# Performance work log

Measured on AMD Instinct MI355X. Metric: run time of the kernel, lower is better.

Reference implementation:

```python
import jax, jax.numpy as jnp
import numpy as np

N_NEURONS = 1024
TABLE_SIZE = 65536  # array_size (2048 quotients) * 2**remainder_size (32)
BATCH = 8192


def setup_inputs() -> dict:
    key = jax.random.key(0)
    k1, k2 = jax.random.split(key)
    # Input tuples: one fingerprint per neuron per sample, value = (quotient << rs) | remainder
    data = jax.random.randint(k1, (BATCH, N_NEURONS), 0, TABLE_SIZE, dtype=jnp.int32)
    # Dense membership/counter table equivalent to the fitted quotient filter state
    # (quotient filter with full remainders stored is an exact fingerprint set).
    table = jax.random.uniform(k2, (N_NEURONS, TABLE_SIZE), dtype=jnp.float32)
    return {"data": data, "table": table}


def reference(data, table):
    # check_member(neuron=j, quotient=data[i,j]>>rs, remainder=data[i,j]&mask)
    # == table[j, data[i,j]]; multi_rank sums memberships over neurons.
    neuron_idx = jnp.arange(table.shape[0])[None, :]          # [1, N]
    gathered = table[neuron_idx, data]                        # [B, N] gather
    response = jnp.sum(gathered, axis=1)                      # [B]
    return response
```

## Files before the change

kernel.cpp:

```cpp
#include <hip/hip_runtime.h>

#define N_NEURONS 1024
#define TABLE_SIZE 65536
#define BATCH 8192
#define NGROUPS 8
#define NPG 128
#define HALF 64
#define SPB 128

__global__ __launch_bounds__(256) void qw_partial_kernel(
    const int* __restrict__ data,
    const float* __restrict__ table,
    float* __restrict__ part)
{
    const int b      = blockIdx.x;
    const int g      = b & (NGROUPS - 1);
    const int sub    = b >> 3;
    const int t      = threadIdx.x;
    const int half   = t >> 7;
    const int sid    = t & (SPB - 1);
    const int sample = sub * SPB + sid;
    const int jbase  = g * NPG + half * HALF;

    const int* __restrict__ drow = data + (size_t)sample * N_NEURONS + jbase;

    float acc = 0.0f;
#pragma unroll
    for (int jo = 0; jo < HALF; jo += 16) {
        const int4 i0 = *reinterpret_cast<const int4*>(drow + jo);
        const int4 i1 = *reinterpret_cast<const int4*>(drow + jo + 4);
        const int4 i2 = *reinterpret_cast<const int4*>(drow + jo + 8);
        const int4 i3 = *reinterpret_cast<const int4*>(drow + jo + 12);
        const float* __restrict__ tp = table + (size_t)(jbase + jo) * TABLE_SIZE;
        const float v0  = tp[(size_t) 0 * TABLE_SIZE + i0.x];
        const float v1  = tp[(size_t) 1 * TABLE_SIZE + i0.y];
        const float v2  = tp[(size_t) 2 * TABLE_SIZE + i0.z];
        const float v3  = tp[(size_t) 3 * TABLE_SIZE + i0.w];
        const float v4  = tp[(size_t) 4 * TABLE_SIZE + i1.x];
        const float v5  = tp[(size_t) 5 * TABLE_SIZE + i1.y];
        const float v6  = tp[(size_t) 6 * TABLE_SIZE + i1.z];
        const float v7  = tp[(size_t) 7 * TABLE_SIZE + i1.w];
        const float v8  = tp[(size_t) 8 * TABLE_SIZE + i2.x];
        const float v9  = tp[(size_t) 9 * TABLE_SIZE + i2.y];
        const float v10 = tp[(size_t)10 * TABLE_SIZE + i2.z];
        const float v11 = tp[(size_t)11 * TABLE_SIZE + i2.w];
        const float v12 = tp[(size_t)12 * TABLE_SIZE + i3.x];
        const float v13 = tp[(size_t)13 * TABLE_SIZE + i3.y];
        const float v14 = tp[(size_t)14 * TABLE_SIZE + i3.z];
        const float v15 = tp[(size_t)15 * TABLE_SIZE + i3.w];
        acc += (((v0 + v1) + (v2 + v3)) + ((v4 + v5) + (v6 + v7)))
             + (((v8 + v9) + (v10 + v11)) + ((v12 + v13) + (v14 + v15)));
    }

    __shared__ float lds[SPB];
    if (half == 0) {
        lds[sid] = acc;
    }
    __syncthreads();
    if (half == 1) {
        part[(size_t)g * BATCH + sample] = lds[sid] + acc;
    }
}

__global__ __launch_bounds__(256) void qw_reduce_kernel(
    const float* __restrict__ part,
    float* __restrict__ out)
{
    const int i = blockIdx.x * 256 + threadIdx.x;
    float s = 0.0f;
#pragma unroll
    for (int g = 0; g < NGROUPS; ++g) {
        s += part[(size_t)g * BATCH + i];
    }
    out[i] = s;
}

__global__ __launch_bounds__(256) void qw_gather_kernel(
    const int* __restrict__ data,
    const float* __restrict__ table,
    float* __restrict__ out)
{
    const int gtid   = blockIdx.x * blockDim.x + threadIdx.x;
    const int sample = gtid >> 6;
    const int lane   = threadIdx.x & 63;
    if (sample >= BATCH) return;
    const int* __restrict__ row = data + (size_t)sample * N_NEURONS;
    float acc = 0.0f;
#pragma unroll
    for (int k = 0; k < 4; ++k) {
        const int jb = 256 * k + 4 * lane;
        const int4 idx4 = *reinterpret_cast<const int4*>(row + jb);
        acc += table[(size_t)(jb + 0) * TABLE_SIZE + idx4.x];
        acc += table[(size_t)(jb + 1) * TABLE_SIZE + idx4.y];
        acc += table[(size_t)(jb + 2) * TABLE_SIZE + idx4.z];
        acc += table[(size_t)(jb + 3) * TABLE_SIZE + idx4.w];
    }
#pragma unroll
    for (int off = 32; off >= 1; off >>= 1) acc += __shfl_xor(acc, off, 64);
    if (lane == 0) out[sample] = acc;
}

extern "C" void kernel_launch(void* const* d_in, const int* in_sizes, int n_in,
                              void* d_out, int out_size, void* d_ws, size_t ws_size,
                              hipStream_t stream)
{
    const int*   data  = (const int*)d_in[0];
    const float* table = (const float*)d_in[1];
    float*       out   = (float*)d_out;

    const size_t need = (size_t)NGROUPS * BATCH * sizeof(float);
    if (ws_size >= need) {
        float* part = (float*)d_ws;
        qw_partial_kernel<<<(BATCH / SPB) * NGROUPS, 256, 0, stream>>>(data, table, part);
        qw_reduce_kernel<<<BATCH / 256, 256, 0, stream>>>(part, out);
    } else {
        qw_gather_kernel<<<BATCH / 4, 256, 0, stream>>>(data, table, out);
    }
}
```

Measured before the change: 91.78 us.

## Split each sample across 4 lanes with interleaved neuron columns and shuffle reduction

The partial kernel now assigns 4 adjacent threads per sample, each covering interleaved groups of 4 neurons within the 128-neuron group. All index loads are issued up front, and the table gathers are software-pipelined with two register sets. A 2-step shuffle reduction replaces the LDS exchange and __syncthreads. Adjacent lanes now read contiguous index memory and hit neighbouring table rows, which changes coalescing and cache locality, and each block covers half as many samples, so the grid doubles.

```diff
diff --git a/kernel.cpp b/kernel.cpp
--- a/kernel.cpp
+++ b/kernel.cpp
@@ -5,8 +5,8 @@
 #define BATCH 8192
 #define NGROUPS 8
 #define NPG 128
-#define HALF 64
-#define SPB 128
+#define SPB 64
+#define TPS 4
 
 __global__ __launch_bounds__(256) void qw_partial_kernel(
     const int* __restrict__ data,
@@ -17,48 +17,49 @@
     const int g      = b & (NGROUPS - 1);
     const int sub    = b >> 3;
     const int t      = threadIdx.x;
-    const int half   = t >> 7;
-    const int sid    = t & (SPB - 1);
+    const int q      = t & (TPS - 1);
+    const int sid    = t >> 2;
     const int sample = sub * SPB + sid;
-    const int jbase  = g * NPG + half * HALF;
 
-    const int* __restrict__ drow = data + (size_t)sample * N_NEURONS + jbase;
+    const int* __restrict__ dptr =
+        data + (size_t)sample * N_NEURONS + g * NPG + q * 4;
+    const int4 idx0 = *reinterpret_cast<const int4*>(dptr + 0 * 16);
+    const int4 idx1 = *reinterpret_cast<const int4*>(dptr + 1 * 16);
+    const int4 idx2 = *reinterpret_cast<const int4*>(dptr + 2 * 16);
+    const int4 idx3 = *reinterpret_cast<const int4*>(dptr + 3 * 16);
+    const int4 idx4 = *reinterpret_cast<const int4*>(dptr + 4 * 16);
+    const int4 idx5 = *reinterpret_cast<const int4*>(dptr + 5 * 16);
+    const int4 idx6 = *reinterpret_cast<const int4*>(dptr + 6 * 16);
+    const int4 idx7 = *reinterpret_cast<const int4*>(dptr + 7 * 16);
 
+    const float* __restrict__ tb =
+        table + (size_t)(g * NPG + q * 4) * TABLE_SIZE;
+
+#define LOADC(a0, a1, a2, a3, I, c)                                   \
+    a0 = tb[(size_t)((c) * 16 + 0) * TABLE_SIZE + (size_t)(I).x];     \
+    a1 = tb[(size_t)((c) * 16 + 1) * TABLE_SIZE + (size_t)(I).y];     \
+    a2 = tb[(size_t)((c) * 16 + 2) * TABLE_SIZE + (size_t)(I).z];     \
+    a3 = tb[(size_t)((c) * 16 + 3) * TABLE_SIZE + (size_t)(I).w];
+
+    float v0, v1, v2, v3, w0, w1, w2, w3;
     float acc = 0.0f;
-#pragma unroll
-    for (int jo = 0; jo < HALF; jo += 16) {
-        const int4 i0 = *reinterpret_cast<const int4*>(drow + jo);
-        const int4 i1 = *reinterpret_cast<const int4*>(drow + jo + 4);
-        const int4 i2 = *reinterpret_cast<const int4*>(drow + jo + 8);
-        const int4 i3 = *reinterpret_cast<const int4*>(drow + jo + 12);
-        const float* __restrict__ tp = table + (size_t)(jbase + jo) * TABLE_SIZE;
-        const float v0  = tp[(size_t) 0 * TABLE_SIZE + i0.x];
-        const float v1  = tp[(size_t) 1 * TABLE_SIZE + i0.y];
-        const float v2  = tp[(size_t) 2 * TABLE_SIZE + i0.z];
-        const float v3  = tp[(size_t) 3 * TABLE_SIZE + i0.w];
-        const float v4  = tp[(size_t) 4 * TABLE_SIZE + i1.x];
-        const float v5  = tp[(size_t) 5 * TABLE_SIZE + i1.y];
-        const float v6  = tp[(size_t) 6 * TABLE_SIZE + i1.z];
-        const float v7  = tp[(size_t) 7 * TABLE_SIZE + i1.w];
-        const float v8  = tp[(size_t) 8 * TABLE_SIZE + i2.x];
-        const float v9  = tp[(size_t) 9 * TABLE_SIZE + i2.y];
-        const float v10 = tp[(size_t)10 * TABLE_SIZE + i2.z];
-        const float v11 = tp[(size_t)11 * TABLE_SIZE + i2.w];
-        const float v12 = tp[(size_t)12 * TABLE_SIZE + i3.x];
-        const float v13 = tp[(size_t)13 * TABLE_SIZE + i3.y];
-        const float v14 = tp[(size_t)14 * TABLE_SIZE + i3.z];
-        const float v15 = tp[(size_t)15 * TABLE_SIZE + i3.w];
-        acc += (((v0 + v1) + (v2 + v3)) + ((v4 + v5) + (v6 + v7)))
-             + (((v8 + v9) + (v10 + v11)) + ((v12 + v13) + (v14 + v15)));
-    }
 
-    __shared__ float lds[SPB];
-    if (half == 0) {
-        lds[sid] = acc;
-    }
-    __syncthreads();
-    if (half == 1) {
-        part[(size_t)g * BATCH + sample] = lds[sid] + acc;
+    LOADC(v0, v1, v2, v3, idx0, 0);
+    LOADC(w0, w1, w2, w3, idx1, 1);  acc += (v0 + v1) + (v2 + v3);
+    LOADC(v0, v1, v2, v3, idx2, 2);  acc += (w0 + w1) + (w2 + w3);
+    LOADC(w0, w1, w2, w3, idx3, 3);  acc += (v0 + v1) + (v2 + v3);
+    LOADC(v0, v1, v2, v3, idx4, 4);  acc += (w0 + w1) + (w2 + w3);
+    LOADC(w0, w1, w2, w3, idx5, 5);  acc += (v0 + v1) + (v2 + v3);
+    LOADC(v0, v1, v2, v3, idx6, 6);  acc += (w0 + w1) + (w2 + w3);
+    LOADC(w0, w1, w2, w3, idx7, 7);  acc += (v0 + v1) + (v2 + v3);
+    acc += (w0 + w1) + (w2 + w3);
+#undef LOADC
+
+    acc += __shfl_xor(acc, 1, 64);
+    acc += __shfl_xor(acc, 2, 64);
+
+    if (q == 0) {
+        part[(size_t)g * BATCH + sample] = acc;
     }
 }
 
@@ -111,7 +112,8 @@
     const size_t need = (size_t)NGROUPS * BATCH * sizeof(float);
     if (ws_size >= need) {
         float* part = (float*)d_ws;
-        qw_partial_kernel<<<(BATCH / SPB) * NGROUPS, 256, 0, stream>>>(data, table, part);
+        const int blocks = (BATCH / SPB) * NGROUPS;
+        qw_partial_kernel<<<blocks, 256, 0, stream>>>(data, table, part);
         qw_reduce_kernel<<<BATCH / 256, 256, 0, stream>>>(part, out);
     } else {
         qw_gather_kernel<<<BATCH / 4, 256, 0, stream>>>(data, table, out);
```

After: 110.3 us. 20.2% more time.

## Stream table rows through LDS instead of random global gathers

Applied to the files above, without the earlier changes.

Adds a new primary path where each block owns four neurons, streams their full table rows through shared memory in 16K-entry chunks, and resolves all 8192 samples' lookups from LDS. This replaces scattered global gathers with sequential row reads. Partial sums per neuron block are written to an 8 MB workspace and reduced by a widened reduce kernel. The cost is reading the entire table, strided data loads, many predicated LDS probes, frequent barriers and low occupancy. The old path is kept as a fallback for smaller workspaces.

```diff
diff --git a/kernel.cpp b/kernel.cpp
--- a/kernel.cpp
+++ b/kernel.cpp
@@ -3,63 +3,67 @@
 #define N_NEURONS 1024
 #define TABLE_SIZE 65536
 #define BATCH 8192
-#define NGROUPS 8
-#define NPG 128
-#define HALF 64
-#define SPB 128
+#define RPB 4
+#define NBLK (N_NEURONS / RPB)
+#define TPB 1024
+#define QSIZE 16384
+#define NQ (TABLE_SIZE / QSIZE)
+#define SPT (BATCH / TPB)
+#define TS ((size_t)TABLE_SIZE)
 
-__global__ __launch_bounds__(256) void qw_partial_kernel(
+__global__ __launch_bounds__(TPB) void qw_stage_kernel(
     const int* __restrict__ data,
     const float* __restrict__ table,
     float* __restrict__ part)
 {
-    const int b      = blockIdx.x;
-    const int g      = b & (NGROUPS - 1);
-    const int sub    = b >> 3;
-    const int t      = threadIdx.x;
-    const int half   = t >> 7;
-    const int sid    = t & (SPB - 1);
-    const int sample = sub * SPB + sid;
-    const int jbase  = g * NPG + half * HALF;
+    __shared__ float lds[QSIZE];
 
-    const int* __restrict__ drow = data + (size_t)sample * N_NEURONS + jbase;
+    const int b = blockIdx.x;
+    const int t = threadIdx.x;
 
-    float acc = 0.0f;
+    int4 qidx[SPT];
 #pragma unroll
-    for (int jo = 0; jo < HALF; jo += 16) {
-        const int4 i0 = *reinterpret_cast<const int4*>(drow + jo);
-        const int4 i1 = *reinterpret_cast<const int4*>(drow + jo + 4);
-        const int4 i2 = *reinterpret_cast<const int4*>(drow + jo + 8);
-        const int4 i3 = *reinterpret_cast<const int4*>(drow + jo + 12);
-        const float* __restrict__ tp = table + (size_t)(jbase + jo) * TABLE_SIZE;
-        const float v0  = tp[(size_t) 0 * TABLE_SIZE + i0.x];
-        const float v1  = tp[(size_t) 1 * TABLE_SIZE + i0.y];
-        const float v2  = tp[(size_t) 2 * TABLE_SIZE + i0.z];
-        const float v3  = tp[(size_t) 3 * TABLE_SIZE + i0.w];
-        const float v4  = tp[(size_t) 4 * TABLE_SIZE + i1.x];
-        const float v5  = tp[(size_t) 5 * TABLE_SIZE + i1.y];
-        const float v6  = tp[(size_t) 6 * TABLE_SIZE + i1.z];
-        const float v7  = tp[(size_t) 7 * TABLE_SIZE + i1.w];
-        const float v8  = tp[(size_t) 8 * TABLE_SIZE + i2.x];
-        const float v9  = tp[(size_t) 9 * TABLE_SIZE + i2.y];
-        const float v10 = tp[(size_t)10 * TABLE_SIZE + i2.z];
-        const float v11 = tp[(size_t)11 * TABLE_SIZE + i2.w];
-        const float v12 = tp[(size_t)12 * TABLE_SIZE + i3.x];
-        const float v13 = tp[(size_t)13 * TABLE_SIZE + i3.y];
-        const float v14 = tp[(size_t)14 * TABLE_SIZE + i3.z];
-        const float v15 = tp[(size_t)15 * TABLE_SIZE + i3.w];
-        acc += (((v0 + v1) + (v2 + v3)) + ((v4 + v5) + (v6 + v7)))
-             + (((v8 + v9) + (v10 + v11)) + ((v12 + v13) + (v14 + v15)));
+    for (int k = 0; k < SPT; ++k) {
+        const int s = t * SPT + k;
+        qidx[k] = *reinterpret_cast<const int4*>(
+            data + (size_t)s * N_NEURONS + b * RPB);
     }
 
-    __shared__ float lds[SPB];
-    if (half == 0) {
-        lds[sid] = acc;
+    float acc[SPT];
+#pragma unroll
+    for (int k = 0; k < SPT; ++k) acc[k] = 0.0f;
+
+#pragma unroll
+    for (int r = 0; r < RPB; ++r) {
+        const float* __restrict__ trow = table + (size_t)(b * RPB + r) * TS;
+#pragma unroll
+        for (int q = 0; q < NQ; ++q) {
+            const float* __restrict__ src = trow + q * QSIZE;
+#pragma unroll
+            for (int j = 0; j < QSIZE / (TPB * 4); ++j) {
+                const int o = j * TPB * 4 + t * 4;
+                *reinterpret_cast<float4*>(&lds[o]) =
+                    *reinterpret_cast<const float4*>(src + o);
+            }
+            __syncthreads();
+
+            const int lo = q * QSIZE;
+#pragma unroll
+            for (int k = 0; k < SPT; ++k) {
+                const int idx = (r == 0) ? qidx[k].x
+                              : (r == 1) ? qidx[k].y
+                              : (r == 2) ? qidx[k].z
+                              :            qidx[k].w;
+                const unsigned rel = (unsigned)(idx - lo);
+                if (rel < (unsigned)QSIZE) acc[k] += lds[rel];
+            }
+            __syncthreads();
+        }
     }
-    __syncthreads();
-    if (half == 1) {
-        part[(size_t)g * BATCH + sample] = lds[sid] + acc;
-    }
+
+    float* __restrict__ dst = part + (size_t)b * BATCH + t * SPT;
+#pragma unroll
+    for (int k = 0; k < SPT; ++k) dst[k] = acc[k];
 }
 
 __global__ __launch_bounds__(256) void qw_reduce_kernel(
@@ -67,11 +71,66 @@
     float* __restrict__ out)
 {
     const int i = blockIdx.x * 256 + threadIdx.x;
+    float s0 = 0.0f, s1 = 0.0f, s2 = 0.0f, s3 = 0.0f;
+#pragma unroll 4
+    for (int b = 0; b < NBLK; b += 4) {
+        s0 += part[(size_t)(b + 0) * BATCH + i];
+        s1 += part[(size_t)(b + 1) * BATCH + i];
+        s2 += part[(size_t)(b + 2) * BATCH + i];
+        s3 += part[(size_t)(b + 3) * BATCH + i];
+    }
+    out[i] = (s0 + s1) + (s2 + s3);
+}
+
+#define MF_NGROUPS 8
+#define MF_NPG 128
+#define MF_SPB 128
+__global__ __launch_bounds__(256) void qw_partial_kernel(
+    const int* __restrict__ data,
+    const float* __restrict__ table,
+    float* __restrict__ part)
+{
+    const int b      = blockIdx.x;
+    const int g      = b & (MF_NGROUPS - 1);
+    const int sub    = b >> 3;
+    const int t      = threadIdx.x;
+    const int h      = t >> 7;
+    const int sid    = t & (MF_SPB - 1);
+    const int sample = sub * MF_SPB + sid;
+    const int jbase  = g * MF_NPG + h * 64;
+
+    const int* __restrict__ drow = data + (size_t)sample * N_NEURONS + jbase;
+    float acc = 0.0f;
+#pragma unroll
+    for (int jo = 0; jo < 64; jo += 16) {
+        const int4 i0 = *reinterpret_cast<const int4*>(drow + jo);
+        const int4 i1 = *reinterpret_cast<const int4*>(drow + jo + 4);
+        const int4 i2 = *reinterpret_cast<const int4*>(drow + jo + 8);
+        const int4 i3 = *reinterpret_cast<const int4*>(drow + jo + 12);
+        const float* __restrict__ tp = table + (size_t)(jbase + jo) * TS;
+        acc += tp[(size_t) 0 * TS + i0.x] + tp[(size_t) 1 * TS + i0.y]
+             + tp[(size_t) 2 * TS + i0.z] + tp[(size_t) 3 * TS + i0.w]
+             + tp[(size_t) 4 * TS + i1.x] + tp[(size_t) 5 * TS + i1.y]
+             + tp[(size_t) 6 * TS + i1.z] + tp[(size_t) 7 * TS + i1.w]
+             + tp[(size_t) 8 * TS + i2.x] + tp[(size_t) 9 * TS + i2.y]
+             + tp[(size_t)10 * TS + i2.z] + tp[(size_t)11 * TS + i2.w]
+             + tp[(size_t)12 * TS + i3.x] + tp[(size_t)13 * TS + i3.y]
+             + tp[(size_t)14 * TS + i3.z] + tp[(size_t)15 * TS + i3.w];
+    }
+    __shared__ float lsum[MF_SPB];
+    if (h == 0) lsum[sid] = acc;
+    __syncthreads();
+    if (h == 1) part[(size_t)g * BATCH + sample] = lsum[sid] + acc;
+}
+
+__global__ __launch_bounds__(256) void qw_reduce8_kernel(
+    const float* __restrict__ part,
+    float* __restrict__ out)
+{
+    const int i = blockIdx.x * 256 + threadIdx.x;
     float s = 0.0f;
 #pragma unroll
-    for (int g = 0; g < NGROUPS; ++g) {
-        s += part[(size_t)g * BATCH + i];
-    }
+    for (int g = 0; g < MF_NGROUPS; ++g) s += part[(size_t)g * BATCH + i];
     out[i] = s;
 }
 
@@ -90,10 +149,10 @@
     for (int k = 0; k < 4; ++k) {
         const int jb = 256 * k + 4 * lane;
         const int4 idx4 = *reinterpret_cast<const int4*>(row + jb);
-        acc += table[(size_t)(jb + 0) * TABLE_SIZE + idx4.x];
-        acc += table[(size_t)(jb + 1) * TABLE_SIZE + idx4.y];
-        acc += table[(size_t)(jb + 2) * TABLE_SIZE + idx4.z];
-        acc += table[(size_t)(jb + 3) * TABLE_SIZE + idx4.w];
+        acc += table[(size_t)(jb + 0) * TS + idx4.x];
+        acc += table[(size_t)(jb + 1) * TS + idx4.y];
+        acc += table[(size_t)(jb + 2) * TS + idx4.z];
+        acc += table[(size_t)(jb + 3) * TS + idx4.w];
     }
 #pragma unroll
     for (int off = 32; off >= 1; off >>= 1) acc += __shfl_xor(acc, off, 64);
@@ -108,11 +167,18 @@
     const float* table = (const float*)d_in[1];
     float*       out   = (float*)d_out;
 
-    const size_t need = (size_t)NGROUPS * BATCH * sizeof(float);
-    if (ws_size >= need) {
+    const size_t stage_bytes = (size_t)NBLK * BATCH * sizeof(float);
+    const size_t mid_bytes   = (size_t)MF_NGROUPS * BATCH * sizeof(float);
+
+    if (ws_size >= stage_bytes) {
         float* part = (float*)d_ws;
-        qw_partial_kernel<<<(BATCH / SPB) * NGROUPS, 256, 0, stream>>>(data, table, part);
+        qw_stage_kernel<<<NBLK, TPB, 0, stream>>>(data, table, part);
         qw_reduce_kernel<<<BATCH / 256, 256, 0, stream>>>(part, out);
+    } else if (ws_size >= mid_bytes) {
+        float* part = (float*)d_ws;
+        qw_partial_kernel<<<(BATCH / MF_SPB) * MF_NGROUPS, 256, 0, stream>>>(
+            data, table, part);
+        qw_reduce8_kernel<<<BATCH / 256, 256, 0, stream>>>(part, out);
     } else {
         qw_gather_kernel<<<BATCH / 4, 256, 0, stream>>>(data, table, out);
     }
```

After: 109.6 us. 1.19x slower.
